# Kernel tuning notes

Measured on AMD Instinct MI355X. Metric: run time of the kernel, lower is better.

The kernel has to match this reference:

```python
import jax, jax.numpy as jnp
import numpy as np

EMBED_DIM = 1024
BATCH = 4
SEQ = 2048


def setup_inputs() -> dict:
    key = jax.random.key(0)
    ks = jax.random.split(key, 9)
    E = EMBED_DIM
    s = 1.0 / np.sqrt(E)
    inp = {
        "x": jax.random.normal(ks[0], (BATCH, SEQ, E), dtype=jnp.float32),
        "Wq": jax.random.uniform(ks[1], (E, E), jnp.float32, -s, s),
        "bq": jax.random.uniform(ks[2], (E,), jnp.float32, -s, s),
        "Wk": jax.random.uniform(ks[3], (E, E), jnp.float32, -s, s),
        "bk": jax.random.uniform(ks[4], (E,), jnp.float32, -s, s),
        "Wv": jax.random.uniform(ks[5], (E, E), jnp.float32, -s, s),
        "bv": jax.random.uniform(ks[6], (E,), jnp.float32, -s, s),
        "Wo": jax.random.uniform(ks[7], (E, E), jnp.float32, -s, s),
        "bo": jax.random.uniform(ks[8], (E,), jnp.float32, -s, s),
    }
    return inp


def reference(x, Wq, bq, Wk, bk, Wv, bv, Wo, bo):
    # x: [B, S, E]. Single-head attention over full embed_dim.
    scale = x.shape[-1] ** -0.5
    q = jnp.einsum("bse,ef->bsf", x, Wq.T) + bq
    k = jnp.einsum("bse,ef->bsf", x, Wk.T) + bk
    v = jnp.einsum("bse,ef->bsf", x, Wv.T) + bv
    scores = jnp.einsum("bqe,bke->bqk", q, k) * scale  # [B, S, S]
    attn = jax.nn.softmax(scores, axis=-1)             # dropout p=0 -> identity
    out = jnp.einsum("bqk,bke->bqe", attn, v)
    return jnp.einsum("bse,ef->bsf", out, Wo.T) + bo
```

## Files before the change

kernel.cpp:

```cpp
#include <hip/hip_runtime.h>
#include <hip/hip_bf16.h>


typedef __bf16 bf16_t;
typedef __bf16 bf16x8 __attribute__((ext_vector_type(8)));
typedef __bf16 bf16x4 __attribute__((ext_vector_type(4)));
typedef float  f32x16 __attribute__((ext_vector_type(16)));
typedef float  f32x4  __attribute__((ext_vector_type(4)));

__device__ __forceinline__ void async_copy16(const void* g, void* l) {
  __builtin_amdgcn_global_load_lds(
      (const __attribute__((address_space(1))) void*)g,
      (__attribute__((address_space(3))) void*)l, 16, 0, 0);
}

__device__ __forceinline__ void wg_barrier() {
  asm volatile("" ::: "memory");
  __builtin_amdgcn_s_barrier();
  asm volatile("" ::: "memory");
}

#define LGKM(n)                                                  \
  do {                                                           \
    asm volatile("s_waitcnt lgkmcnt(" #n ")" ::: "memory");      \
    __builtin_amdgcn_sched_barrier(0);                           \
  } while (0)

#define VM(n) asm volatile("s_waitcnt vmcnt(" #n ")" ::: "memory")

__device__ __forceinline__ unsigned lds_addr(const void* p) {
  return (unsigned)(unsigned long long)(__attribute__((address_space(3))) const void*)p;
}

__device__ __forceinline__ bf16x8 ds_read128(const bf16_t* p) {
  bf16x8 r;
  asm volatile("ds_read_b128 %0, %1" : "=v"(r) : "v"(lds_addr(p)));
  return r;
}

__device__ __forceinline__ f32x4 mfma16(bf16x8 a, bf16x8 b, f32x4 c) {
  return __builtin_amdgcn_mfma_f32_16x16x32_bf16(a, b, c, 0, 0, 0);
}

__device__ __forceinline__ void store_out(float* p, float v)  { *p = v; }
__device__ __forceinline__ void store_out(bf16_t* p, float v) { *p = (bf16_t)v; }

#define BM 128
#define BN 128
#define BKT 64

#define G_AQ(i, ro, bb, co)                                                   \
  acc[(ro) + (i)][(co) + 0] = mfma16(a[i][0], bb[0][0], acc[(ro) + (i)][(co) + 0]); \
  acc[(ro) + (i)][(co) + 1] = mfma16(a[i][0], bb[1][0], acc[(ro) + (i)][(co) + 1]); \
  acc[(ro) + (i)][(co) + 0] = mfma16(a[i][1], bb[0][1], acc[(ro) + (i)][(co) + 0]); \
  acc[(ro) + (i)][(co) + 1] = mfma16(a[i][1], bb[1][1], acc[(ro) + (i)][(co) + 1]);

#define G_BQ(j, bb, co)                                              \
  acc[0][(co) + (j)] = mfma16(a[0][0], bb[j][0], acc[0][(co) + (j)]); \
  acc[1][(co) + (j)] = mfma16(a[1][0], bb[j][0], acc[1][(co) + (j)]); \
  acc[2][(co) + (j)] = mfma16(a[2][0], bb[j][0], acc[2][(co) + (j)]); \
  acc[3][(co) + (j)] = mfma16(a[3][0], bb[j][0], acc[3][(co) + (j)]); \
  acc[0][(co) + (j)] = mfma16(a[0][1], bb[j][1], acc[0][(co) + (j)]); \
  acc[1][(co) + (j)] = mfma16(a[1][1], bb[j][1], acc[1][(co) + (j)]); \
  acc[2][(co) + (j)] = mfma16(a[2][1], bb[j][1], acc[2][(co) + (j)]); \
  acc[3][(co) + (j)] = mfma16(a[3][1], bb[j][1], acc[3][(co) + (j)]);

template <typename OutT, int NBIAS>
__global__ __launch_bounds__(512, 2) void gemm256_bt(
    const bf16_t* __restrict__ A, const bf16_t* __restrict__ B,
    OutT* __restrict__ C,
    const float* __restrict__ b0, const float* __restrict__ b1,
    const float* __restrict__ b2,
    int M, int N, int K, int lda, int ldb, int ldc, float scale,
    long long strideA, long long strideB, long long strideC) {
  const int z = blockIdx.z;
  A += (long long)z * strideA;
  B += (long long)z * strideB;
  C += (long long)z * strideC;

  int bx = blockIdx.x, by = blockIdx.y;
  {
    const int GX  = gridDim.x;
    const int id  = by * GX + bx;
    const int per = GX * 8;
    const int grp = id / per;
    const int rem = id - grp * per;
    by = grp * 8 + (rem & 7);
    bx = rem >> 3;
  }

  __shared__ __align__(16) bf16_t As[2 * 256 * 64];
  __shared__ __align__(16) bf16_t Bs[2 * 256 * 64];

  const int t    = threadIdx.x;
  const int lane = t & 63;
  const int w    = t >> 6;
  const int wm   = w & 1;
  const int wn   = w >> 1;
  const int g    = lane >> 4;
  const int l7   = lane & 7;
  const int r15  = lane & 15;
  const int tileM = by * 256;
  const int tileN = bx * 256;

  const int row0 = t >> 3;
  const int gcc  = (t & 7) ^ (row0 & 7);
  const int dstb = (t & ~63) * 8;

  const int sw0 = ((0 + g) ^ l7) * 8;
  const int sw1 = ((4 + g) ^ l7) * 8;
  const int aRow = (wm * 128 + r15) * 64;
  const int bRow = (wn * 64 + r15) * 64;

  const int NT = K >> 6;

  f32x4 acc[8][4] = {};

  auto stageA = [&](int kt, int h) {
    const int cb = (kt & 1) * 16384;
    const bf16_t* src =
        A + (long long)(tileM + h * 128 + row0) * lda + kt * 64 + gcc * 8;
    bf16_t* dst = &As[cb + h * 8192 + dstb];
    async_copy16(src, dst);
    async_copy16(src + (long long)64 * lda, dst + 4096);
  };
  auto stageB = [&](int kt, int h) {
    const int cb = (kt & 1) * 16384;
    const bf16_t* src =
        B + (long long)(tileN + h * 128 + row0) * ldb + kt * 64 + gcc * 8;
    bf16_t* dst = &Bs[cb + h * 8192 + dstb];
    async_copy16(src, dst);
    async_copy16(src + (long long)64 * ldb, dst + 4096);
  };

  stageA(0, 0); stageA(0, 1); stageB(0, 0); stageB(0, 1);
  VM(0);
  wg_barrier();

  bf16x8 a[4][2], P[2][2], Q[2][2];
#pragma unroll
  for (int j = 0; j < 2; ++j) {
    P[j][0] = ds_read128(&Bs[bRow + j * 1024 + sw0]);
    P[j][1] = ds_read128(&Bs[bRow + j * 1024 + sw1]);
  }

  auto tile_step = [&](int kt, bf16x8 (&bc)[2][2], bf16x8 (&bq)[2][2]) {
    const int cb = (kt & 1) * 16384;
    const int kn = kt + 1;
    const bf16_t* Ab = &As[cb + aRow];
    const bf16_t* Bb = &Bs[cb + bRow];

#pragma unroll
    for (int i = 0; i < 4; ++i) {
      a[i][0] = ds_read128(Ab + i * 1024 + sw0);
      a[i][1] = ds_read128(Ab + i * 1024 + sw1);
    }
    if (kn < NT) { stageB(kn, 0); stageB(kn, 1); }
    __builtin_amdgcn_s_setprio(1);
    LGKM(6);
    G_AQ(0, 0, bc, 0)
    LGKM(4);
    G_AQ(1, 0, bc, 0)
    LGKM(2);
    G_AQ(2, 0, bc, 0)
    LGKM(0);
    G_AQ(3, 0, bc, 0)
    __builtin_amdgcn_s_setprio(0);

#pragma unroll
    for (int j = 0; j < 2; ++j) {
      bq[j][0] = ds_read128(Bb + 2048 + j * 1024 + sw0);
      bq[j][1] = ds_read128(Bb + 2048 + j * 1024 + sw1);
    }
    if (kn < NT) { stageA(kn, 0); stageA(kn, 1); }
    __builtin_amdgcn_s_setprio(1);
    LGKM(2);
    G_BQ(0, bq, 2)
    LGKM(0);
    G_BQ(1, bq, 2)
    __builtin_amdgcn_s_setprio(0);

#pragma unroll
    for (int i = 0; i < 4; ++i) {
      a[i][0] = ds_read128(Ab + 4096 + i * 1024 + sw0);
      a[i][1] = ds_read128(Ab + 4096 + i * 1024 + sw1);
    }
    __builtin_amdgcn_s_setprio(1);
    LGKM(6);
    G_AQ(0, 4, bq, 2)
    LGKM(4);
    G_AQ(1, 4, bq, 2)
    LGKM(2);
    G_AQ(2, 4, bq, 2)
    LGKM(0);
    G_AQ(3, 4, bq, 2)
    __builtin_amdgcn_s_setprio(0);
    VM(0);
    wg_barrier();

    if (kn < NT) {
      const bf16_t* Bn = &Bs[(kn & 1) * 16384 + bRow];
#pragma unroll
      for (int j = 0; j < 2; ++j) {
        bq[j][0] = ds_read128(Bn + j * 1024 + sw0);
        bq[j][1] = ds_read128(Bn + j * 1024 + sw1);
      }
    }
    __builtin_amdgcn_s_setprio(1);
    G_AQ(0, 4, bc, 0)
    G_AQ(1, 4, bc, 0)
    G_AQ(2, 4, bc, 0)
    G_AQ(3, 4, bc, 0)
    __builtin_amdgcn_s_setprio(0);
  };

  for (int kt = 0; kt < NT; kt += 2) {
    tile_step(kt,     P, Q);
    tile_step(kt + 1, Q, P);
  }

  float bvv[4];
#pragma unroll
  for (int j = 0; j < 4; ++j) {
    const int col = tileN + wn * 64 + j * 16 + r15;
    float bv = 0.f;
    if (NBIAS == 1) bv = b0[col];
    if (NBIAS == 3) {
      const float* bp = col < 1024 ? b0 : (col < 2048 ? b1 : b2);
      bv = bp[col & 1023];
    }
    bvv[j] = bv;
  }
#pragma unroll
  for (int i = 0; i < 8; ++i) {
#pragma unroll
    for (int r = 0; r < 4; ++r) {
      const long long row = tileM + wm * 128 + i * 16 + g * 4 + r;
      OutT* Crow = C + row * ldc + tileN + wn * 64 + r15;
#pragma unroll
      for (int j = 0; j < 4; ++j)
        store_out(Crow + j * 16, acc[i][j][r] * scale + bvv[j]);
    }
  }
}

template <typename OutT, int NBIAS>
__global__ __launch_bounds__(256, 2) void gemm128_bt2(
    const bf16_t* __restrict__ A, const bf16_t* __restrict__ B,
    OutT* __restrict__ C,
    const float* __restrict__ b0,
    int M, int N, int K, int lda, int ldb, int ldc, float scale,
    long long strideA, long long strideB, long long strideC) {
  const int z = blockIdx.z;
  A += (long long)z * strideA;
  B += (long long)z * strideB;
  C += (long long)z * strideC;

  int bx = blockIdx.x, by = blockIdx.y;
  {
    const int GX  = gridDim.x;
    const int id  = by * GX + bx;
    const int per = GX * 8;
    const int grp = id / per;
    const int rem = id - grp * per;
    by = grp * 8 + (rem & 7);
    bx = rem >> 3;
  }

  __shared__ __align__(16) bf16_t As[2 * 128 * 64];
  __shared__ __align__(16) bf16_t Bs[2 * 128 * 64];

  const int t    = threadIdx.x;
  const int lane = t & 63;
  const int w    = t >> 6;
  const int wm   = w & 1;
  const int wn   = w >> 1;
  const int g    = lane >> 4;
  const int l7   = lane & 7;
  const int r15  = lane & 15;
  const int tileM = by * 128;
  const int tileN = bx * 128;

  const int sw0 = ((0 + g) ^ l7) * 8;
  const int sw1 = ((4 + g) ^ l7) * 8;
  const int aRow = (wm * 64 + r15) * 64;
  const int bRow = (wn * 64 + r15) * 64;

  const int NT = K >> 6;

  f32x4 acc[4][4] = {};

  auto stageA = [&](int kt) {
    const int cb = (kt & 1) * 8192;
#pragma unroll
    for (int i = 0; i < 4; ++i) {
      const int c   = t + 256 * i;
      const int row = c >> 3;
      const int cc  = c & 7;
      const int gcc = cc ^ (row & 7);
      const int ldsbase = ((t & ~63) + 256 * i) * 8;
      async_copy16(A + (long long)(tileM + row) * lda + kt * 64 + gcc * 8,
                   &As[cb + ldsbase]);
    }
  };
  auto stageB = [&](int kt) {
    const int cb = (kt & 1) * 8192;
#pragma unroll
    for (int i = 0; i < 4; ++i) {
      const int c   = t + 256 * i;
      const int row = c >> 3;
      const int cc  = c & 7;
      const int gcc = cc ^ (row & 7);
      const int ldsbase = ((t & ~63) + 256 * i) * 8;
      async_copy16(B + (long long)(tileN + row) * ldb + kt * 64 + gcc * 8,
                   &Bs[cb + ldsbase]);
    }
  };

  stageA(0); stageB(0);
  VM(0);
  wg_barrier();

  bf16x8 a[2][2], P[2][2], Q[2][2];
#pragma unroll
  for (int j = 0; j < 2; ++j) {
    P[j][0] = ds_read128(&Bs[bRow + j * 1024 + sw0]);
    P[j][1] = ds_read128(&Bs[bRow + j * 1024 + sw1]);
  }

  auto tile_step = [&](int kt, bf16x8 (&bc)[2][2], bf16x8 (&bq)[2][2]) {
    const int cb = (kt & 1) * 8192;
    const int kn = kt + 1;
    const bf16_t* Ab = &As[cb + aRow];
    const bf16_t* Bb = &Bs[cb + bRow];

    a[0][0] = ds_read128(Ab + sw0);
    a[0][1] = ds_read128(Ab + sw1);
    a[1][0] = ds_read128(Ab + 1024 + sw0);
    a[1][1] = ds_read128(Ab + 1024 + sw1);
    if (kn < NT) stageB(kn);
    __builtin_amdgcn_s_setprio(1);
    LGKM(3);
    acc[0][0] = mfma16(a[0][0], bc[0][0], acc[0][0]);
    acc[0][1] = mfma16(a[0][0], bc[1][0], acc[0][1]);
    LGKM(2);
    acc[0][0] = mfma16(a[0][1], bc[0][1], acc[0][0]);
    acc[0][1] = mfma16(a[0][1], bc[1][1], acc[0][1]);
    LGKM(1);
    acc[1][0] = mfma16(a[1][0], bc[0][0], acc[1][0]);
    acc[1][1] = mfma16(a[1][0], bc[1][0], acc[1][1]);
    LGKM(0);
    acc[1][0] = mfma16(a[1][1], bc[0][1], acc[1][0]);
    acc[1][1] = mfma16(a[1][1], bc[1][1], acc[1][1]);
    __builtin_amdgcn_s_setprio(0);

    bq[0][0] = ds_read128(Bb + 2048 + sw0);
    bq[0][1] = ds_read128(Bb + 2048 + sw1);
    bq[1][0] = ds_read128(Bb + 3072 + sw0);
    bq[1][1] = ds_read128(Bb + 3072 + sw1);
    if (kn < NT) stageA(kn);
    __builtin_amdgcn_s_setprio(1);
    LGKM(3);
    acc[0][2] = mfma16(a[0][0], bq[0][0], acc[0][2]);
    acc[1][2] = mfma16(a[1][0], bq[0][0], acc[1][2]);
    LGKM(2);
    acc[0][2] = mfma16(a[0][1], bq[0][1], acc[0][2]);
    acc[1][2] = mfma16(a[1][1], bq[0][1], acc[1][2]);
    LGKM(1);
    acc[0][3] = mfma16(a[0][0], bq[1][0], acc[0][3]);
    acc[1][3] = mfma16(a[1][0], bq[1][0], acc[1][3]);
    LGKM(0);
    acc[0][3] = mfma16(a[0][1], bq[1][1], acc[0][3]);
    acc[1][3] = mfma16(a[1][1], bq[1][1], acc[1][3]);
    __builtin_amdgcn_s_setprio(0);

    a[0][0] = ds_read128(Ab + 2048 + sw0);
    a[0][1] = ds_read128(Ab + 2048 + sw1);
    a[1][0] = ds_read128(Ab + 3072 + sw0);
    a[1][1] = ds_read128(Ab + 3072 + sw1);
    __builtin_amdgcn_s_setprio(1);
    LGKM(3);
    acc[2][2] = mfma16(a[0][0], bq[0][0], acc[2][2]);
    acc[2][3] = mfma16(a[0][0], bq[1][0], acc[2][3]);
    LGKM(2);
    acc[2][2] = mfma16(a[0][1], bq[0][1], acc[2][2]);
    acc[2][3] = mfma16(a[0][1], bq[1][1], acc[2][3]);
    LGKM(1);
    acc[3][2] = mfma16(a[1][0], bq[0][0], acc[3][2]);
    acc[3][3] = mfma16(a[1][0], bq[1][0], acc[3][3]);
    LGKM(0);
    acc[3][2] = mfma16(a[1][1], bq[0][1], acc[3][2]);
    acc[3][3] = mfma16(a[1][1], bq[1][1], acc[3][3]);
    __builtin_amdgcn_s_setprio(0);
    VM(0);
    wg_barrier();

    if (kn < NT) {
      const bf16_t* Bn = &Bs[(kn & 1) * 8192 + bRow];
      bq[0][0] = ds_read128(Bn + sw0);
      bq[0][1] = ds_read128(Bn + sw1);
      bq[1][0] = ds_read128(Bn + 1024 + sw0);
      bq[1][1] = ds_read128(Bn + 1024 + sw1);
    }
    __builtin_amdgcn_s_setprio(1);
    acc[2][0] = mfma16(a[0][0], bc[0][0], acc[2][0]);
    acc[2][0] = mfma16(a[0][1], bc[0][1], acc[2][0]);
    acc[2][1] = mfma16(a[0][0], bc[1][0], acc[2][1]);
    acc[2][1] = mfma16(a[0][1], bc[1][1], acc[2][1]);
    acc[3][0] = mfma16(a[1][0], bc[0][0], acc[3][0]);
    acc[3][0] = mfma16(a[1][1], bc[0][1], acc[3][0]);
    acc[3][1] = mfma16(a[1][0], bc[1][0], acc[3][1]);
    acc[3][1] = mfma16(a[1][1], bc[1][1], acc[3][1]);
    __builtin_amdgcn_s_setprio(0);
  };

  for (int kt = 0; kt < NT; kt += 2) {
    tile_step(kt,     P, Q);
    tile_step(kt + 1, Q, P);
  }

  float bvv[4];
#pragma unroll
  for (int j = 0; j < 4; ++j) {
    const int col = tileN + wn * 64 + j * 16 + r15;
    bvv[j] = (NBIAS == 1) ? b0[col] : 0.f;
  }
#pragma unroll
  for (int i = 0; i < 4; ++i) {
#pragma unroll
    for (int r = 0; r < 4; ++r) {
      const long long row = tileM + wm * 64 + i * 16 + g * 4 + r;
      OutT* Crow = C + row * ldc + tileN + wn * 64 + r15;
#pragma unroll
      for (int j = 0; j < 4; ++j)
        store_out(Crow + j * 16, acc[i][j][r] * scale + bvv[j]);
    }
  }
}

template <typename OutT, int NBIAS>
__global__ __launch_bounds__(256) void gemm_bt(
    const bf16_t* __restrict__ A, const bf16_t* __restrict__ B,
    OutT* __restrict__ C,
    const float* __restrict__ b0, const float* __restrict__ b1,
    const float* __restrict__ b2,
    int M, int N, int K, int lda, int ldb, int ldc, float scale,
    long long strideA, long long strideB, long long strideC) {
  const int z = blockIdx.z;
  A += (long long)z * strideA;
  B += (long long)z * strideB;
  C += (long long)z * strideC;

  int bx = blockIdx.x, by = blockIdx.y;
  {
    const int GX  = gridDim.x;
    const int id  = by * GX + bx;
    const int per = GX * 8;
    const int grp = id / per;
    const int rem = id - grp * per;
    by = grp * 8 + (rem & 7);
    bx = rem >> 3;
  }

  __shared__ __align__(16) bf16_t As[BM * BKT];
  __shared__ __align__(16) bf16_t Bs[BN * BKT];

  const int t    = threadIdx.x;
  const int lane = t & 63;
  const int w    = t >> 6;
  const int wm   = w & 1;
  const int wn   = w >> 1;
  const int tileM = by * BM;
  const int tileN = bx * BN;

  f32x16 acc[2][2] = {};

  for (int k0 = 0; k0 < K; k0 += BKT) {
#pragma unroll
    for (int i = 0; i < 4; ++i) {
      const int c   = t + 256 * i;
      const int row = c >> 3;
      const int cc  = c & 7;
      const int gcc = cc ^ (row & 7);
      const int ldsbase = ((t & ~63) + 256 * i) * 8;
      async_copy16(A + (long long)(tileM + row) * lda + k0 + gcc * 8, &As[ldsbase]);
      async_copy16(B + (long long)(tileN + row) * ldb + k0 + gcc * 8, &Bs[ldsbase]);
    }
    __syncthreads();

#pragma unroll
    for (int s = 0; s < 4; ++s) {
      const int kc = s + 4 * (lane >> 5);
      bf16x8 af[2], bfr[2];
#pragma unroll
      for (int ti = 0; ti < 2; ++ti) {
        const int row = wm * 64 + ti * 32 + (lane & 31);
        af[ti] = *(const bf16x8*)&As[row * BKT + ((kc ^ (row & 7)) * 8)];
      }
#pragma unroll
      for (int tj = 0; tj < 2; ++tj) {
        const int row = wn * 64 + tj * 32 + (lane & 31);
        bfr[tj] = *(const bf16x8*)&Bs[row * BKT + ((kc ^ (row & 7)) * 8)];
      }
#pragma unroll
      for (int ti = 0; ti < 2; ++ti)
#pragma unroll
        for (int tj = 0; tj < 2; ++tj)
          acc[ti][tj] = __builtin_amdgcn_mfma_f32_32x32x16_bf16(
              af[ti], bfr[tj], acc[ti][tj], 0, 0, 0);
    }
    __syncthreads();
  }

#pragma unroll
  for (int tj = 0; tj < 2; ++tj) {
    const int col = tileN + wn * 64 + tj * 32 + (lane & 31);
    float bv = 0.f;
    if (NBIAS == 1) bv = b0[col];
    if (NBIAS == 3) {
      const float* bp = col < 1024 ? b0 : (col < 2048 ? b1 : b2);
      bv = bp[col & 1023];
    }
#pragma unroll
    for (int ti = 0; ti < 2; ++ti) {
      const int rowb = tileM + wm * 64 + ti * 32 + 4 * (lane >> 5);
#pragma unroll
      for (int r = 0; r < 16; ++r) {
        const int row = rowb + (r & 3) + 8 * (r >> 2);
        store_out(&C[(long long)row * ldc + col], acc[ti][tj][r] * scale + bv);
      }
    }
  }
}

__global__ __launch_bounds__(256) void cast_all(
    const float4* __restrict__ w0, const float4* __restrict__ w1,
    const float4* __restrict__ w2, const float4* __restrict__ w3,
    const float4* __restrict__ x,
    bf16x4* __restrict__ d0, bf16x4* __restrict__ d1,
    bf16x4* __restrict__ d2, bf16x4* __restrict__ d3,
    bf16x4* __restrict__ xdst) {
  const int N4W = 1 << 18;
  const int id = blockIdx.x * 256 + threadIdx.x;
  const float4* src;
  bf16x4* dst;
  if (id < 4 * N4W) {
    const int z = id >> 18;
    const int i = id & (N4W - 1);
    src = (z == 0 ? w0 : z == 1 ? w1 : z == 2 ? w2 : w3) + i;
    dst = (z == 0 ? d0 : z == 1 ? d1 : z == 2 ? d2 : d3) + i;
  } else {
    const int i = id - 4 * N4W;
    src = x + i;
    dst = xdst + i;
  }
  const float4 v = *src;
  bf16x4 o;
  o[0] = (bf16_t)v.x; o[1] = (bf16_t)v.y; o[2] = (bf16_t)v.z; o[3] = (bf16_t)v.w;
  *dst = o;
}

__global__ __launch_bounds__(256) void bias_v(
    const bf16_t* __restrict__ WkT, const float* __restrict__ bq,
    float* __restrict__ v) {
  const int wv   = threadIdx.x >> 6;
  const int lane = threadIdx.x & 63;
  const int j    = blockIdx.x * 4 + wv;
  const bf16x8* row = (const bf16x8*)(WkT + (long long)j * 1024);
  float acc = 0.f;
#pragma unroll
  for (int h = 0; h < 2; ++h) {
    const bf16x8 w8 = row[lane * 2 + h];
#pragma unroll
    for (int e = 0; e < 8; ++e)
      acc += (float)w8[e] * bq[lane * 16 + h * 8 + e];
  }
#pragma unroll
  for (int off = 32; off > 0; off >>= 1) acc += __shfl_xor(acc, off);
  if (lane == 0) v[j] = acc;
}

__global__ __launch_bounds__(256) void transpose_bf16(
    const bf16_t* __restrict__ in, bf16_t* __restrict__ out, int R, int C,
    int ldin, long long sIn, long long sOut) {
  in  += (long long)blockIdx.z * sIn;
  out += (long long)blockIdx.z * sOut;
  __shared__ bf16_t tile[32][33];
  const int tx = threadIdx.x, ty = threadIdx.y;
  const int x = blockIdx.x * 32 + tx;
  const int y0 = blockIdx.y * 32;
#pragma unroll
  for (int j = 0; j < 32; j += 8)
    tile[ty + j][tx] = in[(long long)(y0 + ty + j) * ldin + x];
  __syncthreads();
  const int x2 = y0 + tx;
  const int y2 = blockIdx.x * 32;
#pragma unroll
  for (int j = 0; j < 32; j += 8)
    out[(long long)(y2 + ty + j) * R + x2] = tile[tx][ty + j];
}

__global__ __launch_bounds__(256) void softmax_rows(
    const bf16_t* __restrict__ S, bf16_t* __restrict__ P, int cols) {
  const long long row = blockIdx.x;
  const bf16x8* inp = (const bf16x8*)(S + row * cols);
  bf16x8* outp      = (bf16x8*)(P + row * cols);
  const int t = threadIdx.x;
  const int w = t >> 6, lane = t & 63;

  const bf16x8 v = inp[t];
  float f[8];
#pragma unroll
  for (int j = 0; j < 8; ++j) f[j] = (float)v[j];

  float m = f[0];
#pragma unroll
  for (int j = 1; j < 8; ++j) m = fmaxf(m, f[j]);
#pragma unroll
  for (int off = 32; off > 0; off >>= 1) m = fmaxf(m, __shfl_xor(m, off));

  __shared__ float red[8];
  if (lane == 0) red[w] = m;
  __syncthreads();
  m = fmaxf(fmaxf(red[0], red[1]), fmaxf(red[2], red[3]));

  float e[8], sum = 0.f;
#pragma unroll
  for (int j = 0; j < 8; ++j) { e[j] = __expf(f[j] - m); sum += e[j]; }
#pragma unroll
  for (int off = 32; off > 0; off >>= 1) sum += __shfl_xor(sum, off);
  if (lane == 0) red[4 + w] = sum;
  __syncthreads();
  sum = red[4] + red[5] + red[6] + red[7];

  const float inv = 1.f / sum;
  bf16x8 o;
#pragma unroll
  for (int j = 0; j < 8; ++j) o[j] = (bf16_t)(e[j] * inv);
  outp[t] = o;
}

extern "C" void kernel_launch(void* const* d_in, const int* in_sizes, int n_in,
                              void* d_out, int out_size, void* d_ws, size_t ws_size,
                              hipStream_t stream) {
  const int E = 1024, S = 2048, B = 4;
  const int BS = B * S;

  const float* x  = (const float*)d_in[0];
  const float* Wq = (const float*)d_in[1];
  const float* bq = (const float*)d_in[2];
  const float* Wk = (const float*)d_in[3];
  const float* bk = (const float*)d_in[4];
  const float* Wv = (const float*)d_in[5];
  const float* bv = (const float*)d_in[6];
  const float* Wo = (const float*)d_in[7];
  const float* bo = (const float*)d_in[8];
  float* out = (float*)d_out;
  (void)bk; (void)Wk;

  char* w = (char*)d_ws;
  const size_t MB = 1ull << 20;
  bf16_t* Wqb  = (bf16_t*)(w + 0 * MB);
  bf16_t* Wkb  = Wqb + E * E;
  bf16_t* Wob  = (bf16_t*)(w + 4 * MB);
  float*  vb   = (float*)(w + 6 * MB);
  bf16_t* xb   = (bf16_t*)(w + 8 * MB);
  bf16_t* QVb  = (bf16_t*)(w + 24 * MB);
  bf16_t* WqTb = (bf16_t*)(w + 56 * MB);
  bf16_t* WkTb = WqTb + E * E;
  bf16_t* Wqv  = (bf16_t*)(w + 60 * MB);
  bf16_t* Wvb  = Wqv + E * E;
  bf16_t* VTb  = (bf16_t*)(w + 72 * MB);
  bf16_t* Sb   = (bf16_t*)(w + 88 * MB);
  bf16_t* Pb   = (bf16_t*)(w + 8 * MB);
  bf16_t* Ob   = (bf16_t*)(w + 40 * MB);

  {
    const int totalBlocks = ((4 << 18) + (1 << 21)) / 256;
    cast_all<<<totalBlocks, 256, 0, stream>>>(
        (const float4*)Wq, (const float4*)Wk, (const float4*)Wv,
        (const float4*)Wo, (const float4*)x,
        (bf16x4*)Wqb, (bf16x4*)Wkb, (bf16x4*)Wvb, (bf16x4*)Wob, (bf16x4*)xb);
  }

  transpose_bf16<<<dim3(E / 32, E / 32, 2), dim3(32, 8), 0, stream>>>(
      Wqb, WqTb, E, E, E, (long long)E * E, (long long)E * E);

  bias_v<<<256, 256, 0, stream>>>(WkTb, bq, vb);

  gemm_bt<bf16_t, 0><<<dim3(E / BN, E / BM, 1), 256, 0, stream>>>(
      WkTb, WqTb, Wqv, nullptr, nullptr, nullptr,
      E, E, E, E, E, E, 1.f, 0, 0, 0);

  gemm256_bt<bf16_t, 3><<<dim3(2 * E / 256, BS / 256, 1), 512, 0, stream>>>(
      xb, Wqv, QVb, vb, bv, bv,
      BS, 2 * E, E, E, E, 2 * E, 1.f, 0, 0, 0);

  transpose_bf16<<<dim3(E / 32, S / 32, B), dim3(32, 8), 0, stream>>>(
      QVb + E, VTb, S, E, 2 * E, (long long)S * 2 * E, (long long)E * S);

  gemm256_bt<bf16_t, 0><<<dim3(S / 256, S / 256, B), 512, 0, stream>>>(
      QVb, xb, Sb, nullptr, nullptr, nullptr,
      S, S, E, 2 * E, E, S, 0.03125f,
      (long long)S * 2 * E, (long long)S * E, (long long)S * S);

  softmax_rows<<<BS, 256, 0, stream>>>(Sb, Pb, S);

  gemm128_bt2<bf16_t, 0><<<dim3(E / 128, S / 128, B), 256, 0, stream>>>(
      Pb, VTb, Ob, nullptr,
      S, E, S, S, S, E, 1.f,
      (long long)S * S, (long long)E * S, (long long)S * E);

  gemm128_bt2<float, 1><<<dim3(E / 128, BS / 128, 1), 256, 0, stream>>>(
      Ob, Wob, out, bo,
      BS, E, E, E, E, E, 1.f, 0, 0, 0);
}
```

Before: 281.5 us.

## Split-K the weight-product GEMM and retile scores GEMM to 128x128

Replaces the dedicated 128x128 gemm_bt used for the small Wk^T·Wq weight product with a split-K (two halves of K=512) launch of gemm128_bt2 writing fp32 partials, followed by a combine kernel that sums and casts to bf16. This doubles the block count for a 1024x1024 GEMM that otherwise fills only 64 workgroups. The Q·X^T scores GEMM also switches from the 256x256 kernel to the 128x128 kernel, trading per-block reuse for more blocks. It adds an extra kernel launch and 8 MB of fp32 partial traffic.

New measurement: 273.8 us. 1.03x faster.

```diff
diff --git a/kernel.cpp b/kernel.cpp
--- a/kernel.cpp
+++ b/kernel.cpp
@@ -44,10 +44,6 @@
 
 __device__ __forceinline__ void store_out(float* p, float v)  { *p = v; }
 __device__ __forceinline__ void store_out(bf16_t* p, float v) { *p = (bf16_t)v; }
-
-#define BM 128
-#define BN 128
-#define BKT 64
 
 #define G_AQ(i, ro, bb, co)                                                   \
   acc[(ro) + (i)][(co) + 0] = mfma16(a[i][0], bb[0][0], acc[(ro) + (i)][(co) + 0]); \
@@ -438,99 +434,15 @@
   }
 }
 
-template <typename OutT, int NBIAS>
-__global__ __launch_bounds__(256) void gemm_bt(
-    const bf16_t* __restrict__ A, const bf16_t* __restrict__ B,
-    OutT* __restrict__ C,
-    const float* __restrict__ b0, const float* __restrict__ b1,
-    const float* __restrict__ b2,
-    int M, int N, int K, int lda, int ldb, int ldc, float scale,
-    long long strideA, long long strideB, long long strideC) {
-  const int z = blockIdx.z;
-  A += (long long)z * strideA;
-  B += (long long)z * strideB;
-  C += (long long)z * strideC;
-
-  int bx = blockIdx.x, by = blockIdx.y;
-  {
-    const int GX  = gridDim.x;
-    const int id  = by * GX + bx;
-    const int per = GX * 8;
-    const int grp = id / per;
-    const int rem = id - grp * per;
-    by = grp * 8 + (rem & 7);
-    bx = rem >> 3;
-  }
-
-  __shared__ __align__(16) bf16_t As[BM * BKT];
-  __shared__ __align__(16) bf16_t Bs[BN * BKT];
-
-  const int t    = threadIdx.x;
-  const int lane = t & 63;
-  const int w    = t >> 6;
-  const int wm   = w & 1;
-  const int wn   = w >> 1;
-  const int tileM = by * BM;
-  const int tileN = bx * BN;
-
-  f32x16 acc[2][2] = {};
-
-  for (int k0 = 0; k0 < K; k0 += BKT) {
-#pragma unroll
-    for (int i = 0; i < 4; ++i) {
-      const int c   = t + 256 * i;
-      const int row = c >> 3;
-      const int cc  = c & 7;
-      const int gcc = cc ^ (row & 7);
-      const int ldsbase = ((t & ~63) + 256 * i) * 8;
-      async_copy16(A + (long long)(tileM + row) * lda + k0 + gcc * 8, &As[ldsbase]);
-      async_copy16(B + (long long)(tileN + row) * ldb + k0 + gcc * 8, &Bs[ldsbase]);
-    }
-    __syncthreads();
-
-#pragma unroll
-    for (int s = 0; s < 4; ++s) {
-      const int kc = s + 4 * (lane >> 5);
-      bf16x8 af[2], bfr[2];
-#pragma unroll
-      for (int ti = 0; ti < 2; ++ti) {
-        const int row = wm * 64 + ti * 32 + (lane & 31);
-        af[ti] = *(const bf16x8*)&As[row * BKT + ((kc ^ (row & 7)) * 8)];
-      }
-#pragma unroll
-      for (int tj = 0; tj < 2; ++tj) {
-        const int row = wn * 64 + tj * 32 + (lane & 31);
-        bfr[tj] = *(const bf16x8*)&Bs[row * BKT + ((kc ^ (row & 7)) * 8)];
-      }
-#pragma unroll
-      for (int ti = 0; ti < 2; ++ti)
-#pragma unroll
-        for (int tj = 0; tj < 2; ++tj)
-          acc[ti][tj] = __builtin_amdgcn_mfma_f32_32x32x16_bf16(
-              af[ti], bfr[tj], acc[ti][tj], 0, 0, 0);
-    }
-    __syncthreads();
-  }
-
-#pragma unroll
-  for (int tj = 0; tj < 2; ++tj) {
-    const int col = tileN + wn * 64 + tj * 32 + (lane & 31);
-    float bv = 0.f;
-    if (NBIAS == 1) bv = b0[col];
-    if (NBIAS == 3) {
-      const float* bp = col < 1024 ? b0 : (col < 2048 ? b1 : b2);
-      bv = bp[col & 1023];
-    }
-#pragma unroll
-    for (int ti = 0; ti < 2; ++ti) {
-      const int rowb = tileM + wm * 64 + ti * 32 + 4 * (lane >> 5);
-#pragma unroll
-      for (int r = 0; r < 16; ++r) {
-        const int row = rowb + (r & 3) + 8 * (r >> 2);
-        store_out(&C[(long long)row * ldc + col], acc[ti][tj][r] * scale + bv);
-      }
-    }
-  }
+__global__ __launch_bounds__(256) void combine_mt(
+    const float4* __restrict__ p0, const float4* __restrict__ p1,
+    bf16x4* __restrict__ o) {
+  const int id = blockIdx.x * 256 + threadIdx.x;
+  const float4 a = p0[id], b = p1[id];
+  bf16x4 r;
+  r[0] = (bf16_t)(a.x + b.x); r[1] = (bf16_t)(a.y + b.y);
+  r[2] = (bf16_t)(a.z + b.z); r[3] = (bf16_t)(a.w + b.w);
+  o[id] = r;
 }
 
 __global__ __launch_bounds__(256) void cast_all(
@@ -674,6 +586,7 @@
   bf16_t* Sb   = (bf16_t*)(w + 88 * MB);
   bf16_t* Pb   = (bf16_t*)(w + 8 * MB);
   bf16_t* Ob   = (bf16_t*)(w + 40 * MB);
+  float*  MTf  = (float*)(w + 120 * MB);
 
   {
     const int totalBlocks = ((4 << 18) + (1 << 21)) / 256;
@@ -688,9 +601,12 @@
 
   bias_v<<<256, 256, 0, stream>>>(WkTb, bq, vb);
 
-  gemm_bt<bf16_t, 0><<<dim3(E / BN, E / BM, 1), 256, 0, stream>>>(
-      WkTb, WqTb, Wqv, nullptr, nullptr, nullptr,
-      E, E, E, E, E, E, 1.f, 0, 0, 0);
+  gemm128_bt2<float, 0><<<dim3(E / 128, E / 128, 2), 256, 0, stream>>>(
+      WkTb, WqTb, MTf, nullptr,
+      E, E, 512, E, E, E, 1.f, 512, 512, (long long)E * E);
+
+  combine_mt<<<(E * E / 4) / 256, 256, 0, stream>>>(
+      (const float4*)MTf, (const float4*)(MTf + E * E), (bf16x4*)Wqv);
 
   gemm256_bt<bf16_t, 3><<<dim3(2 * E / 256, BS / 256, 1), 512, 0, stream>>>(
       xb, Wqv, QVb, vb, bv, bv,
@@ -699,8 +615,8 @@
   transpose_bf16<<<dim3(E / 32, S / 32, B), dim3(32, 8), 0, stream>>>(
       QVb + E, VTb, S, E, 2 * E, (long long)S * 2 * E, (long long)E * S);
 
-  gemm256_bt<bf16_t, 0><<<dim3(S / 256, S / 256, B), 512, 0, stream>>>(
-      QVb, xb, Sb, nullptr, nullptr, nullptr,
+  gemm128_bt2<bf16_t, 0><<<dim3(S / 128, S / 128, B), 256, 0, stream>>>(
+      QVb, xb, Sb, nullptr,
       S, S, E, 2 * E, E, S, 0.03125f,
       (long long)S * 2 * E, (long long)S * E, (long long)S * S);
 
```
